# Kernel optimization log

Hardware: AMD Instinct MI355X
Metric: run time of the kernel (lower is better)

## Reference

```python
import jax, jax.numpy as jnp
import numpy as np

N, L, D = 4, 4096, 1024
H = 16
HD = D // H          # 64
MLP = 4 * D          # 4096
EPS = 1e-5

def log_g(x):
    # torch: where(x>=0, log(relu(x)+0.5), -softplus(-x))
    return jnp.where(x >= 0.0, jnp.log(jax.nn.relu(x) + 0.5), -jax.nn.softplus(-x))

def parallel_scan_log(log_coeffs, log_values):
    # log_coeffs: (B, L, C); log_values: (B, L+1, C)
    a_star = jnp.pad(jnp.cumsum(log_coeffs, axis=1), ((0, 0), (1, 0), (0, 0)))
    log_h = jax.lax.cumlogsumexp(log_values - a_star, axis=1)
    return jnp.exp(a_star[:, 1:] + log_h[:, 1:])

def layer_norm(x, gamma, beta):
    mu = jnp.mean(x, axis=-1, keepdims=True)
    var = jnp.var(x, axis=-1, keepdims=True)
    return (x - mu) * jax.lax.rsqrt(var + EPS) * gamma + beta

def setup_inputs() -> dict:
    key = jax.random.key(0)
    ks = jax.random.split(key, 12)
    s = 0.02
    return {
        "x": jax.random.normal(ks[0], (N, L, D), jnp.float32),
        "h_0": jax.random.normal(ks[1], (N, 1, D), jnp.float32),
        "w_in": jax.random.normal(ks[2], (D, D), jnp.float32) * s,
        "b_in": jnp.zeros((D,), jnp.float32),
        "wz": jax.random.normal(ks[3], (HD, HD), jnp.float32) * s,
        "bz": jnp.zeros((HD,), jnp.float32),
        "wh": jax.random.normal(ks[4], (HD, HD), jnp.float32) * s,
        "bh": jnp.zeros((HD,), jnp.float32),
        "w_out": jax.random.normal(ks[5], (D, D), jnp.float32) * s,
        "b_out": jnp.zeros((D,), jnp.float32),
        "ln1_g": jnp.ones((D,), jnp.float32),
        "ln1_b": jnp.zeros((D,), jnp.float32),
        "ln2_g": jnp.ones((D,), jnp.float32),
        "ln2_b": jnp.zeros((D,), jnp.float32),
        "mw1": jax.random.normal(ks[6], (D, MLP), jnp.float32) * s,
        "mb1": jnp.zeros((MLP,), jnp.float32),
        "mw2": jax.random.normal(ks[7], (MLP, MLP), jnp.float32) * s,
        "mb2": jnp.zeros((MLP,), jnp.float32),
        "mw3": jax.random.normal(ks[8], (MLP, D), jnp.float32) * s,
        "mb3": jnp.zeros((D,), jnp.float32),
    }

def reference(x, h_0, w_in, b_in, wz, bz, wh, bh, w_out, b_out,
              ln1_g, ln1_b, ln2_g, ln2_b, mw1, mb1, mw2, mb2, mw3, mb3):
    n, l, d = x.shape
    rnn_input = layer_norm(x, ln1_g, ln1_b)
    pi = rnn_input @ w_in + b_in                                 # (N,L,D)
    pi = pi.reshape(n, l, H, HD).transpose(0, 2, 1, 3).reshape(n * H, l, HD)
    h0 = h_0.reshape(n, 1, H, HD).transpose(0, 2, 1, 3).reshape(n * H, 1, HD)
    # minGRU in log-space
    k = pi @ wz + bz
    log_z = -jax.nn.softplus(-k)
    log_coeffs = -jax.nn.softplus(k)
    log_h0 = log_g(h0)
    log_th = log_g(pi @ wh + bh)
    h = parallel_scan_log(log_coeffs, jnp.concatenate([log_h0, log_z + log_th], axis=1))
    rnn_states = h.reshape(n, H, l, HD).transpose(0, 2, 1, 3).reshape(n, l, d)
    x = x + (rnn_states @ w_out + b_out)
    mlp_in = layer_norm(x, ln2_g, ln2_b)
    y = jax.nn.silu(mlp_in @ mw1 + mb1)
    y = jax.nn.silu(y @ mw2 + mb2)
    y = y @ mw3 + mb3
    return (x + y, rnn_states)
```

## Files before the change

### kernel.cpp

```cpp
#include <hip/hip_runtime.h>
#include <hip/hip_bf16.h>

typedef __attribute__((ext_vector_type(8))) short short8;
typedef __attribute__((ext_vector_type(4))) short short4v;
typedef __attribute__((ext_vector_type(4))) float f32x4;
using bf16 = __hip_bfloat16;

#define DEV static __device__ __forceinline__

DEV float bf2f(bf16 v) { return __bfloat162float(v); }
DEV bf16 f2bf(float v) { return __float2bfloat16(v); }
DEV float s2f(short s) {
  union { unsigned u; float f; } v;
  v.u = ((unsigned)(unsigned short)s) << 16;
  return v.f;
}
DEV short f2s(float v) {
  bf16 b = __float2bfloat16(v);
  return *(short*)&b;
}

DEV void gld_lds16(const void* g, void* l) {
  __builtin_amdgcn_global_load_lds(
      (const __attribute__((address_space(1))) void*)g,
      (__attribute__((address_space(3))) void*)l, 16, 0, 0);
}

__global__ __launch_bounds__(256)
void wconv_kernel(const float* __restrict__ w, bf16* __restrict__ wT, int K, int N) {
  __shared__ float tile[32][33];
  const int kt = blockIdx.x * 32, nt = blockIdx.y * 32;
  const int tx = threadIdx.x & 31, ty = threadIdx.x >> 5;
#pragma unroll
  for (int i = 0; i < 32; i += 8)
    tile[ty + i][tx] = w[(size_t)(kt + ty + i) * N + nt + tx];
  __syncthreads();
#pragma unroll
  for (int i = 0; i < 32; i += 8)
    wT[(size_t)(nt + ty + i) * K + kt + tx] = f2bf(tile[tx][ty + i]);
}

__global__ __launch_bounds__(256)
void ln_kernel(const float* __restrict__ x, const float* __restrict__ g,
               const float* __restrict__ b, bf16* __restrict__ out) {
  const int row = blockIdx.x;
  const int t = threadIdx.x;
  const float4 v = ((const float4*)(x + (size_t)row * 1024))[t];
  float s = v.x + v.y + v.z + v.w;
  float ss = v.x * v.x + v.y * v.y + v.z * v.z + v.w * v.w;
#pragma unroll
  for (int off = 32; off > 0; off >>= 1) {
    s += __shfl_down(s, off);
    ss += __shfl_down(ss, off);
  }
  __shared__ float red[8];
  if ((t & 63) == 0) { red[(t >> 6) * 2] = s; red[(t >> 6) * 2 + 1] = ss; }
  __syncthreads();
  s = red[0] + red[2] + red[4] + red[6];
  ss = red[1] + red[3] + red[5] + red[7];
  const float mu = s * (1.f / 1024.f);
  const float rstd = rsqrtf(ss * (1.f / 1024.f) - mu * mu + 1e-5f);
  const float4 g4 = ((const float4*)g)[t];
  const float4 b4 = ((const float4*)b)[t];
  struct alignas(8) B4 { bf16 v[4]; } o;
  o.v[0] = f2bf((v.x - mu) * rstd * g4.x + b4.x);
  o.v[1] = f2bf((v.y - mu) * rstd * g4.y + b4.y);
  o.v[2] = f2bf((v.z - mu) * rstd * g4.z + b4.z);
  o.v[3] = f2bf((v.w - mu) * rstd * g4.w + b4.w);
  *(B4*)(out + (size_t)row * 1024 + t * 4) = o;
}

template <int EPI>
__global__ __launch_bounds__(256, 2)
void gemm128(const bf16* __restrict__ A, const bf16* __restrict__ BT,
             const float* __restrict__ bias, const float* __restrict__ res,
             void* __restrict__ C, int M, int N, int K) {
  __shared__ short As[128 * 64];
  __shared__ short Bs[128 * 64];
  const int tid = threadIdx.x;
  const int l = tid & 63;
  const int w = tid >> 6;
  const int wr = w >> 1, wc = w & 1;

  const int nbn = N >> 7;
  const int nwg = gridDim.x;
  const int bid = blockIdx.x;
  const int q = nwg >> 3, r = nwg & 7;
  const int xcd = bid & 7, lin = bid >> 3;
  const int wg = (xcd < r ? xcd * (q + 1) : r * (q + 1) + (xcd - r) * q) + lin;
  const int bm = wg / nbn, bn = wg % nbn;

  const bf16* Ab = A + (size_t)bm * 128 * K;
  const bf16* Bb = BT + (size_t)bn * 128 * K;

  f32x4 acc[4][4];
#pragma unroll
  for (int i = 0; i < 4; ++i)
#pragma unroll
    for (int j = 0; j < 4; ++j) acc[i][j] = (f32x4){0.f, 0.f, 0.f, 0.f};

  const int srow = l >> 3;
  const int scol = (((l & 7) ^ (l >> 3)) << 3);

  for (int k0 = 0; k0 < K; k0 += 64) {
    __syncthreads();
#pragma unroll
    for (int p = 0; p < 4; ++p) {
      const int rowA = p * 32 + w * 8 + srow;
      gld_lds16(Ab + (size_t)rowA * K + k0 + scol, As + (p * 32 + w * 8) * 64);
      gld_lds16(Bb + (size_t)rowA * K + k0 + scol, Bs + (p * 32 + w * 8) * 64);
    }
    __syncthreads();
    const int xr = (l & 7) << 3;
#pragma unroll
    for (int kk = 0; kk < 2; ++kk) {
      short8 fa[4], fb[4];
#pragma unroll
      for (int m = 0; m < 4; ++m)
        fa[m] = *(const short8*)&As[(wr * 64 + m * 16 + (l & 15)) * 64 +
                                    ((kk * 32 + (l >> 4) * 8) ^ xr)];
#pragma unroll
      for (int n = 0; n < 4; ++n)
        fb[n] = *(const short8*)&Bs[(wc * 64 + n * 16 + (l & 15)) * 64 +
                                    ((kk * 32 + (l >> 4) * 8) ^ xr)];
#pragma unroll
      for (int m = 0; m < 4; ++m)
#pragma unroll
        for (int n = 0; n < 4; ++n)
          acc[m][n] = __builtin_amdgcn_mfma_f32_16x16x32_bf16(fa[m], fb[n], acc[m][n], 0, 0, 0);
    }
  }

  const int lc = l & 15;
  const int lr = (l >> 4) * 4;
#pragma unroll
  for (int m = 0; m < 4; ++m) {
    const int row = bm * 128 + wr * 64 + m * 16 + lr;
#pragma unroll
    for (int r2 = 0; r2 < 4; ++r2) {
      const size_t rowoff = (size_t)(row + r2) * N;
#pragma unroll
      for (int n = 0; n < 4; ++n) {
        const int col = bn * 128 + wc * 64 + n * 16 + lc;
        float v = acc[m][n][r2] + bias[col];
        const size_t off = rowoff + col;
        if constexpr (EPI == 1) v = v / (1.f + __expf(-v));
        if constexpr (EPI == 2) {
          ((float*)C)[off] = res[off] + v;
        } else {
          ((bf16*)C)[off] = f2bf(v);
        }
      }
    }
  }
  (void)M;
}

template <int EPI>
__global__ __launch_bounds__(512, 2)
void gemm256(const bf16* __restrict__ A, const bf16* __restrict__ BT,
             const float* __restrict__ bias, const float* __restrict__ res,
             void* __restrict__ C, int M, int N, int K) {
  __shared__ alignas(16) short As[2][256 * 64];
  __shared__ alignas(16) short Bs[2][256 * 64];
  const int tid = threadIdx.x;
  const int l = tid & 63;
  const int w = tid >> 6;
  const int wr = w >> 2;
  const int wc = w & 3;

  const int nbn = N >> 8;
  const int nwg = gridDim.x;
  const int bid = blockIdx.x;
  const int q = nwg >> 3, r = nwg & 7;
  const int xcd = bid & 7, lin = bid >> 3;
  const int wg = (xcd < r ? xcd * (q + 1) : r * (q + 1) + (xcd - r) * q) + lin;
  const int bm = wg / nbn, bn = wg % nbn;

  const bf16* Ab = A + (size_t)bm * 256 * K;
  const bf16* Bb = BT + (size_t)bn * 256 * K;

  const int gcol = ((l & 7) ^ (l >> 3)) << 3;
  const int fr = l & 15;
  const int kq = (l >> 4) << 3;
  const int xr = (l & 7) << 3;
  const int k0s = kq ^ xr;
  const int k1s = (32 + kq) ^ xr;

  const bf16* Abl = Ab + (size_t)(w * 16 + (l >> 3)) * K + gcol;
  const bf16* Bbl = Bb + (size_t)(w * 16 + (l >> 3)) * K + gcol;

  f32x4 acc[8][4];
#pragma unroll
  for (int i = 0; i < 8; ++i)
#pragma unroll
    for (int j = 0; j < 4; ++j) acc[i][j] = (f32x4){0.f, 0.f, 0.f, 0.f};

  short8 fa[2][2];
  short8 fb[4][2];

#define BARX() __builtin_amdgcn_s_barrier()
#define SBAR0() __builtin_amdgcn_sched_barrier(0)

#define STAGE_A(BUF, HALF, KT)                                                     \
  do {                                                                             \
    gld_lds16(Abl + (size_t)((HALF) * 128) * K + (size_t)(KT) * 64,                \
              &As[BUF][((HALF) * 128 + w * 16) * 64]);                             \
    gld_lds16(Abl + (size_t)((HALF) * 128 + 8) * K + (size_t)(KT) * 64,            \
              &As[BUF][((HALF) * 128 + w * 16 + 8) * 64]);                         \
  } while (0)

#define STAGE_B(BUF, HALF, KT)                                                     \
  do {                                                                             \
    gld_lds16(Bbl + (size_t)((HALF) * 128) * K + (size_t)(KT) * 64,                \
              &Bs[BUF][((HALF) * 128 + w * 16) * 64]);                             \
    gld_lds16(Bbl + (size_t)((HALF) * 128 + 8) * K + (size_t)(KT) * 64,            \
              &Bs[BUF][((HALF) * 128 + w * 16 + 8) * 64]);                         \
  } while (0)

#define RD_FA(BUF, Q)                                                                    \
  do {                                                                                  \
    fa[0][0] = *(const short8*)&As[BUF][(wr * 128 + (Q) * 32 + fr) * 64 + k0s];         \
    fa[0][1] = *(const short8*)&As[BUF][(wr * 128 + (Q) * 32 + fr) * 64 + k1s];         \
    fa[1][0] = *(const short8*)&As[BUF][(wr * 128 + (Q) * 32 + 16 + fr) * 64 + k0s];    \
    fa[1][1] = *(const short8*)&As[BUF][(wr * 128 + (Q) * 32 + 16 + fr) * 64 + k1s];    \
  } while (0)

#define RD_FB(BUF)                                                                      \
  do {                                                                                 \
    _Pragma("unroll") for (int n_ = 0; n_ < 4; ++n_) {                                 \
      fb[n_][0] = *(const short8*)&Bs[BUF][(wc * 64 + n_ * 16 + fr) * 64 + k0s];       \
      fb[n_][1] = *(const short8*)&Bs[BUF][(wc * 64 + n_ * 16 + fr) * 64 + k1s];       \
    }                                                                                  \
  } while (0)

#define MMA_Q(Q)                                                                        \
  do {                                                                                 \
    __builtin_amdgcn_s_setprio(1);                                                     \
    _Pragma("unroll") for (int n_ = 0; n_ < 4; ++n_) {                                 \
      acc[2 * (Q)][n_] = __builtin_amdgcn_mfma_f32_16x16x32_bf16(                      \
          fa[0][0], fb[n_][0], acc[2 * (Q)][n_], 0, 0, 0);                             \
      acc[2 * (Q) + 1][n_] = __builtin_amdgcn_mfma_f32_16x16x32_bf16(                  \
          fa[1][0], fb[n_][0], acc[2 * (Q) + 1][n_], 0, 0, 0);                         \
    }                                                                                  \
    _Pragma("unroll") for (int n_ = 0; n_ < 4; ++n_) {                                 \
      acc[2 * (Q)][n_] = __builtin_amdgcn_mfma_f32_16x16x32_bf16(                      \
          fa[0][1], fb[n_][1], acc[2 * (Q)][n_], 0, 0, 0);                             \
      acc[2 * (Q) + 1][n_] = __builtin_amdgcn_mfma_f32_16x16x32_bf16(                  \
          fa[1][1], fb[n_][1], acc[2 * (Q) + 1][n_], 0, 0, 0);                         \
    }                                                                                  \
    __builtin_amdgcn_s_setprio(0);                                                     \
  } while (0)

#define LGKM0() do { asm volatile("s_waitcnt lgkmcnt(0)"); SBAR0(); } while (0)

#define TILE(BUF, T, HASA, HASB)                                                       \
  do {                                                                                 \
                                                                               \
    LGKM0();                                                                           \
    MMA_Q(0);                                                                          \
    if (HASA) { STAGE_A((BUF) ^ 1, 0, (T) + 1); STAGE_A((BUF) ^ 1, 1, (T) + 1); }      \
    RD_FA(BUF, 1);                                                                     \
    SBAR0(); BARX();                                                                   \
                                                                               \
    LGKM0();                                                                           \
    MMA_Q(1);                                                                          \
    RD_FA(BUF, 2);                                                                     \
    SBAR0(); BARX();                                                                   \
                                                                               \
    LGKM0();                                                                           \
    MMA_Q(2);                                                                          \
    if (HASB) STAGE_B(BUF, 0, (T) + 2);                                                \
    if (HASA) {                                                                        \
      if (HASB) asm volatile("s_waitcnt vmcnt(2)" ::: "memory");                       \
      else      asm volatile("s_waitcnt vmcnt(0)" ::: "memory");                       \
    }                                                                                  \
    RD_FA(BUF, 3);                                                                     \
    SBAR0(); BARX();                                                                   \
                                                                               \
    LGKM0();                                                                           \
    MMA_Q(3);                                                                          \
    if (HASB) STAGE_B(BUF, 1, (T) + 2);                                                \
    if (HASA) {                                                                        \
      RD_FB((BUF) ^ 1);                                                                \
      RD_FA((BUF) ^ 1, 0);                                                             \
      SBAR0(); BARX();                                                                 \
    }                                                                                  \
  } while (0)

  STAGE_A(0, 0, 0); STAGE_A(0, 1, 0);
  STAGE_B(0, 0, 0); STAGE_B(0, 1, 0);
  STAGE_B(1, 0, 1); STAGE_B(1, 1, 1);
  asm volatile("s_waitcnt vmcnt(4)" ::: "memory");
  BARX();
  RD_FB(0);
  RD_FA(0, 0);

  const int NT = K >> 6;
  const int NI = NT >> 1;
#pragma unroll 1
  for (int i = 0; i < NI; ++i) {
    const int t0 = 2 * i;
    const bool b0 = (t0 + 2) < NT;
    const bool b1 = (t0 + 3) < NT;
    TILE(0, t0, true, b0);
    TILE(1, t0 + 1, b0, b1);
  }

#undef BARX
#undef SBAR0
#undef STAGE_A
#undef STAGE_B
#undef RD_FA
#undef RD_FB
#undef MMA_Q
#undef LGKM0
#undef TILE

  const int lc = l & 15;
  const int lr = (l >> 4) * 4;
#pragma unroll
  for (int m = 0; m < 8; ++m) {
    const int row = bm * 256 + wr * 128 + m * 16 + lr;
#pragma unroll
    for (int r2 = 0; r2 < 4; ++r2) {
      const size_t rowoff = (size_t)(row + r2) * N;
#pragma unroll
      for (int n = 0; n < 4; ++n) {
        const int col = bn * 256 + wc * 64 + n * 16 + lc;
        float v = acc[m][n][r2] + bias[col];
        const size_t off = rowoff + col;
        if constexpr (EPI == 1) v = v / (1.f + __expf(-v));
        if constexpr (EPI == 2) {
          ((float*)C)[off] = res[off] + v;
        } else {
          ((bf16*)C)[off] = f2bf(v);
        }
      }
    }
  }
  (void)M;
}

__global__ __launch_bounds__(256)
void heads_kernel(const bf16* __restrict__ piB,
                  const float* __restrict__ wz, const float* __restrict__ bz,
                  const float* __restrict__ wh, const float* __restrict__ bh,
                  bf16* __restrict__ aB, bf16* __restrict__ bB,
                  float* __restrict__ cA, float* __restrict__ cB) {
  __shared__ float wzs[4096], whs[4096], pis[4096];
  __shared__ float segA[4][64], segB[4][64];
  const int h = blockIdx.y;
  const int t0 = blockIdx.x * 64;
  const int tid = threadIdx.x;
#pragma unroll
  for (int i = tid; i < 4096; i += 256) {
    wzs[i] = wz[i];
    whs[i] = wh[i];
  }
#pragma unroll
  for (int rr = 0; rr < 4; ++rr) {
    const int v = tid + rr * 256;
    const int row = v >> 4, c4 = (v & 15) * 4;
    short4v p4 = *(const short4v*)(piB + (size_t)(t0 + row) * 1024 + h * 64 + c4);
    pis[row * 64 + c4 + 0] = s2f(p4[0]);
    pis[row * 64 + c4 + 1] = s2f(p4[1]);
    pis[row * 64 + c4 + 2] = s2f(p4[2]);
    pis[row * 64 + c4 + 3] = s2f(p4[3]);
  }
  __syncthreads();
  const int hd = tid & 63;
  const int tb = (tid >> 6) * 16;
  float accK[16], accT[16];
  const float bzv = bz[hd], bhv = bh[hd];
#pragma unroll
  for (int i = 0; i < 16; ++i) { accK[i] = bzv; accT[i] = bhv; }
  for (int j = 0; j < 64; ++j) {
    const float wzv = wzs[j * 64 + hd];
    const float whv = whs[j * 64 + hd];
#pragma unroll
    for (int i = 0; i < 16; ++i) {
      const float p = pis[(tb + i) * 64 + j];
      accK[i] = fmaf(p, wzv, accK[i]);
      accT[i] = fmaf(p, whv, accT[i]);
    }
  }
  float As = 1.f, Bs = 0.f;
#pragma unroll
  for (int i = 0; i < 16; ++i) {
    const float k = accK[i], th = accT[i];
    const float sig = 1.f / (1.f + __expf(-k));
    const float a = 1.f - sig;
    const float gg = th >= 0.f ? th + 0.5f : 1.f / (1.f + __expf(-th));
    const float bb = sig * gg;
    Bs = fmaf(a, Bs, bb);
    As *= a;
    const size_t idx = (size_t)(t0 + tb + i) * 1024 + h * 64 + hd;
    aB[idx] = f2bf(a);
    bB[idx] = f2bf(bb);
  }
  segA[tid >> 6][hd] = As;
  segB[tid >> 6][hd] = Bs;
  __syncthreads();
  if (tid < 64) {
    float A = segA[0][tid], B = segB[0][tid];
#pragma unroll
    for (int s = 1; s < 4; ++s) {
      B = fmaf(segA[s][tid], B, segB[s][tid]);
      A *= segA[s][tid];
    }
    const int n = t0 >> 12;
    const int chunk = (t0 >> 6) & 63;
    const size_t o = ((size_t)(n * 64 + chunk)) * 1024 + h * 64 + tid;
    cA[o] = A;
    cB[o] = B;
  }
}

__global__ __launch_bounds__(256)
void scan_phase2(const float* __restrict__ h0,
                 const float* __restrict__ cA, const float* __restrict__ cB,
                 float* __restrict__ hst) {
  const int idx = blockIdx.x * 256 + threadIdx.x;
  const int c = idx & 1023;
  const int n = idx >> 10;
  float hv = h0[(size_t)n * 1024 + c];
  hv = hv >= 0.f ? hv + 0.5f : 1.f / (1.f + __expf(-hv));
  for (int ch = 0; ch < 64; ++ch) {
    const size_t o = ((size_t)(n * 64 + ch)) * 1024 + c;
    hst[o] = hv;
    hv = fmaf(cA[o], hv, cB[o]);
  }
}

__global__ __launch_bounds__(128)
void scan_phase3(const bf16* __restrict__ aB, const bf16* __restrict__ bB,
                 const float* __restrict__ hst,
                 float* __restrict__ rnn, bf16* __restrict__ rnnB) {
  const int idx = blockIdx.x * 128 + threadIdx.x;
  const int c8 = idx & 127;
  const int chunk = (idx >> 7) & 63;
  const int n = idx >> 13;
  const int c0 = c8 * 8;
  float hv[8];
  const float4* hsrc = (const float4*)(hst + ((size_t)(n * 64 + chunk)) * 1024 + c0);
  float4 ha = hsrc[0], hb = hsrc[1];
  hv[0] = ha.x; hv[1] = ha.y; hv[2] = ha.z; hv[3] = ha.w;
  hv[4] = hb.x; hv[5] = hb.y; hv[6] = hb.z; hv[7] = hb.w;
  size_t base = ((size_t)(n * 4096 + chunk * 64)) * 1024 + c0;
#pragma unroll 4
  for (int s = 0; s < 64; ++s) {
    const short8 a8 = *(const short8*)(aB + base);
    const short8 b8 = *(const short8*)(bB + base);
    short8 ob;
    float4 o0, o1;
#pragma unroll
    for (int j = 0; j < 8; ++j) {
      hv[j] = fmaf(s2f(a8[j]), hv[j], s2f(b8[j]));
      ob[j] = f2s(hv[j]);
    }
    o0.x = hv[0]; o0.y = hv[1]; o0.z = hv[2]; o0.w = hv[3];
    o1.x = hv[4]; o1.y = hv[5]; o1.z = hv[6]; o1.w = hv[7];
    ((float4*)(rnn + base))[0] = o0;
    ((float4*)(rnn + base))[1] = o1;
    *(short8*)(rnnB + base) = ob;
    base += 1024;
  }
}

extern "C" void kernel_launch(void* const* d_in, const int* in_sizes, int n_in,
                              void* d_out, int out_size, void* d_ws, size_t ws_size,
                              hipStream_t stream) {
  const float* x    = (const float*)d_in[0];
  const float* h0   = (const float*)d_in[1];
  const float* w_in = (const float*)d_in[2];
  const float* b_in = (const float*)d_in[3];
  const float* wz   = (const float*)d_in[4];
  const float* bz   = (const float*)d_in[5];
  const float* wh   = (const float*)d_in[6];
  const float* bh   = (const float*)d_in[7];
  const float* w_out= (const float*)d_in[8];
  const float* b_out= (const float*)d_in[9];
  const float* ln1g = (const float*)d_in[10];
  const float* ln1b = (const float*)d_in[11];
  const float* ln2g = (const float*)d_in[12];
  const float* ln2b = (const float*)d_in[13];
  const float* mw1  = (const float*)d_in[14];
  const float* mb1  = (const float*)d_in[15];
  const float* mw2  = (const float*)d_in[16];
  const float* mb2  = (const float*)d_in[17];
  const float* mw3  = (const float*)d_in[18];
  const float* mb3  = (const float*)d_in[19];
  (void)in_sizes; (void)n_in; (void)out_size;

  float* out0 = (float*)d_out;
  float* out1 = (float*)d_out + (size_t)16384 * 1024;

  char* ws = (char*)d_ws;
  size_t o = 0;
  auto take = [&](size_t bytes) { char* p = ws + o; o += (bytes + 255) & ~(size_t)255; return p; };
  bf16* w_inT = (bf16*)take((size_t)1024 * 1024 * 2);
  bf16* w_outT= (bf16*)take((size_t)1024 * 1024 * 2);
  bf16* mw1T  = (bf16*)take((size_t)4096 * 1024 * 2);
  bf16* mw2T  = (bf16*)take((size_t)4096 * 4096 * 2);
  bf16* mw3T  = (bf16*)take((size_t)4096 * 1024 * 2);
  bf16* lnxB  = (bf16*)take((size_t)16384 * 1024 * 2);
  bf16* piB   = (bf16*)take((size_t)16384 * 1024 * 2);
  bf16* aB    = (bf16*)take((size_t)16384 * 1024 * 2);
  bf16* bB    = (bf16*)take((size_t)16384 * 1024 * 2);
  float* cA   = (float*)take((size_t)4 * 64 * 1024 * 4);
  float* cB   = (float*)take((size_t)4 * 64 * 1024 * 4);
  float* hst  = (float*)take((size_t)4 * 64 * 1024 * 4);
  if (o > ws_size) return;

  const size_t bigbuf = (size_t)16384 * 4096 * 2;
  bf16* t1 = aB;
  bf16* t2 = bB;
  bool big = false;
  if (o + 2 * bigbuf <= ws_size) {
    big = true;
    t1 = (bf16*)take(bigbuf);
    t2 = (bf16*)take(bigbuf);
  }

  wconv_kernel<<<dim3(32, 32), 256, 0, stream>>>(w_in, w_inT, 1024, 1024);
  wconv_kernel<<<dim3(32, 32), 256, 0, stream>>>(w_out, w_outT, 1024, 1024);
  wconv_kernel<<<dim3(32, 128), 256, 0, stream>>>(mw1, mw1T, 1024, 4096);
  wconv_kernel<<<dim3(128, 128), 256, 0, stream>>>(mw2, mw2T, 4096, 4096);
  wconv_kernel<<<dim3(128, 32), 256, 0, stream>>>(mw3, mw3T, 4096, 1024);

  ln_kernel<<<16384, 256, 0, stream>>>(x, ln1g, ln1b, lnxB);
  gemm256<0><<<256, 512, 0, stream>>>(lnxB, w_inT, b_in, nullptr, piB, 16384, 1024, 1024);

  heads_kernel<<<dim3(256, 16), 256, 0, stream>>>(piB, wz, bz, wh, bh, aB, bB, cA, cB);
  scan_phase2<<<16, 256, 0, stream>>>(h0, cA, cB, hst);
  scan_phase3<<<256, 128, 0, stream>>>(aB, bB, hst, out1, lnxB );

  gemm256<2><<<256, 512, 0, stream>>>(lnxB, w_outT, b_out, x, out0, 16384, 1024, 1024);

  ln_kernel<<<16384, 256, 0, stream>>>(out0, ln2g, ln2b, lnxB );
  if (big) {
    gemm256<1><<<1024, 512, 0, stream>>>(lnxB, mw1T, mb1, nullptr, t1, 16384, 4096, 1024);
    gemm256<1><<<1024, 512, 0, stream>>>(t1, mw2T, mb2, nullptr, t2, 16384, 4096, 4096);
    gemm128<2><<<1024, 256, 0, stream>>>(t2, mw3T, mb3, out0, out0, 16384, 1024, 4096);
  } else {
    for (int mc = 0; mc < 4; ++mc) {
      const bf16* a3 = lnxB + (size_t)mc * 4096 * 1024;
      gemm256<1><<<256, 512, 0, stream>>>(a3, mw1T, mb1, nullptr, t1, 4096, 4096, 1024);
      gemm256<1><<<256, 512, 0, stream>>>(t1, mw2T, mb2, nullptr, t2, 4096, 4096, 4096);
      float* oc = out0 + (size_t)mc * 4096 * 1024;
      gemm128<2><<<256, 256, 0, stream>>>(t2, mw3T, mb3, oc, oc, 4096, 1024, 4096);
    }
  }
}
```

Before: 1.191 ms.

## Triple-buffer A tiles in GEMM and transpose pi tile in heads kernel

The GEMM now keeps three LDS buffers for A and two for B. Prefetch runs two k-tiles ahead, with A staging spread across quarters and the loop unrolled in six-tile chunks. This is meant to hide global-load latency better, at the cost of 32 KB more LDS per block, which may reduce occupancy below the launch-bound target of 2 blocks per CU. The heads kernel also stores the pi tile transposed and padded so each thread reads 16 timesteps with four float4 LDS loads instead of 16 scalar loads. The new loop structure assumes the tile count fits the chunk and tail pattern, which may not hold for every K.

```diff
diff --git a/kernel.cpp b/kernel.cpp
--- a/kernel.cpp
+++ b/kernel.cpp
@@ -161,7 +161,7 @@
 void gemm256(const bf16* __restrict__ A, const bf16* __restrict__ BT,
              const float* __restrict__ bias, const float* __restrict__ res,
              void* __restrict__ C, int M, int N, int K) {
-  __shared__ alignas(16) short As[2][256 * 64];
+  __shared__ alignas(16) short As[3][256 * 64];
   __shared__ alignas(16) short Bs[2][256 * 64];
   const int tid = threadIdx.x;
   const int l = tid & 63;
@@ -202,19 +202,19 @@
 #define BARX() __builtin_amdgcn_s_barrier()
 #define SBAR0() __builtin_amdgcn_sched_barrier(0)
 
-#define STAGE_A(BUF, HALF, KT)                                                     \
+#define STAGE_A(BUF, HALF, P)                                                      \
   do {                                                                             \
-    gld_lds16(Abl + (size_t)((HALF) * 128) * K + (size_t)(KT) * 64,                \
+    gld_lds16((P) + (size_t)((HALF) * 128) * K,                                    \
               &As[BUF][((HALF) * 128 + w * 16) * 64]);                             \
-    gld_lds16(Abl + (size_t)((HALF) * 128 + 8) * K + (size_t)(KT) * 64,            \
+    gld_lds16((P) + (size_t)((HALF) * 128 + 8) * K,                                \
               &As[BUF][((HALF) * 128 + w * 16 + 8) * 64]);                         \
   } while (0)
 
-#define STAGE_B(BUF, HALF, KT)                                                     \
+#define STAGE_B(BUF, HALF, P)                                                      \
   do {                                                                             \
-    gld_lds16(Bbl + (size_t)((HALF) * 128) * K + (size_t)(KT) * 64,                \
+    gld_lds16((P) + (size_t)((HALF) * 128) * K,                                    \
               &Bs[BUF][((HALF) * 128 + w * 16) * 64]);                             \
-    gld_lds16(Bbl + (size_t)((HALF) * 128 + 8) * K + (size_t)(KT) * 64,            \
+    gld_lds16((P) + (size_t)((HALF) * 128 + 8) * K,                                \
               &Bs[BUF][((HALF) * 128 + w * 16 + 8) * 64]);                         \
   } while (0)
 
@@ -254,58 +254,69 @@
 
 #define LGKM0() do { asm volatile("s_waitcnt lgkmcnt(0)"); SBAR0(); } while (0)
 
-#define TILE(BUF, T, HASA, HASB)                                                       \
+#define TILE3(A0v, A1v, A2v, BSv, BTv, PF, NX)                                         \
   do {                                                                                 \
                                                                                \
     LGKM0();                                                                           \
     MMA_Q(0);                                                                          \
-    if (HASA) { STAGE_A((BUF) ^ 1, 0, (T) + 1); STAGE_A((BUF) ^ 1, 1, (T) + 1); }      \
-    RD_FA(BUF, 1);                                                                     \
+    if (PF) STAGE_A(A2v, 0, pfA);                                                      \
+    RD_FA(A0v, 1);                                                                     \
     SBAR0(); BARX();                                                                   \
                                                                                \
     LGKM0();                                                                           \
     MMA_Q(1);                                                                          \
-    RD_FA(BUF, 2);                                                                     \
+    if (PF) STAGE_A(A2v, 1, pfA);                                                      \
+    RD_FA(A0v, 2);                                                                     \
     SBAR0(); BARX();                                                                   \
                                                                                \
     LGKM0();                                                                           \
     MMA_Q(2);                                                                          \
-    if (HASB) STAGE_B(BUF, 0, (T) + 2);                                                \
-    if (HASA) {                                                                        \
-      if (HASB) asm volatile("s_waitcnt vmcnt(2)" ::: "memory");                       \
-      else      asm volatile("s_waitcnt vmcnt(0)" ::: "memory");                       \
+    if (PF) {                                                                          \
+      STAGE_B(BSv, 0, pfB);                                                            \
+      asm volatile("s_waitcnt vmcnt(6)" ::: "memory");                                 \
+    } else if (NX) {                                                                   \
+      asm volatile("s_waitcnt vmcnt(0)" ::: "memory");                                 \
     }                                                                                  \
-    RD_FA(BUF, 3);                                                                     \
+    RD_FA(A0v, 3);                                                                     \
     SBAR0(); BARX();                                                                   \
                                                                                \
     LGKM0();                                                                           \
     MMA_Q(3);                                                                          \
-    if (HASB) STAGE_B(BUF, 1, (T) + 2);                                                \
-    if (HASA) {                                                                        \
-      RD_FB((BUF) ^ 1);                                                                \
-      RD_FA((BUF) ^ 1, 0);                                                             \
+    if (PF) STAGE_B(BSv, 1, pfB);                                                      \
+    if (NX) {                                                                          \
+      RD_FB(BTv);                                                                      \
+      RD_FA(A1v, 0);                                                                   \
       SBAR0(); BARX();                                                                 \
     }                                                                                  \
+    if (PF) { pfA += 64; pfB += 64; }                                                  \
   } while (0)
 
-  STAGE_A(0, 0, 0); STAGE_A(0, 1, 0);
-  STAGE_B(0, 0, 0); STAGE_B(0, 1, 0);
-  STAGE_B(1, 0, 1); STAGE_B(1, 1, 1);
-  asm volatile("s_waitcnt vmcnt(4)" ::: "memory");
+  STAGE_A(0, 0, Abl); STAGE_A(0, 1, Abl);
+  STAGE_B(0, 0, Bbl); STAGE_B(0, 1, Bbl);
+  STAGE_A(1, 0, Abl + 64); STAGE_A(1, 1, Abl + 64);
+  STAGE_B(1, 0, Bbl + 64); STAGE_B(1, 1, Bbl + 64);
+  asm volatile("s_waitcnt vmcnt(8)" ::: "memory");
   BARX();
   RD_FB(0);
   RD_FA(0, 0);
 
   const int NT = K >> 6;
-  const int NI = NT >> 1;
+  const int nch = (NT - 4) / 6;
+  const bf16* pfA = Abl + 2 * 64;
+  const bf16* pfB = Bbl + 2 * 64;
 #pragma unroll 1
-  for (int i = 0; i < NI; ++i) {
-    const int t0 = 2 * i;
-    const bool b0 = (t0 + 2) < NT;
-    const bool b1 = (t0 + 3) < NT;
-    TILE(0, t0, true, b0);
-    TILE(1, t0 + 1, b0, b1);
-  }
+  for (int ch = 0; ch < nch; ++ch) {
+    TILE3(0, 1, 2, 0, 1, true, true);
+    TILE3(1, 2, 0, 1, 0, true, true);
+    TILE3(2, 0, 1, 0, 1, true, true);
+    TILE3(0, 1, 2, 1, 0, true, true);
+    TILE3(1, 2, 0, 0, 1, true, true);
+    TILE3(2, 0, 1, 1, 0, true, true);
+  }
+  TILE3(0, 1, 2, 0, 1, true, true);
+  TILE3(1, 2, 0, 1, 0, true, true);
+  TILE3(2, 0, 1, 0, 1, false, true);
+  TILE3(0, 1, 2, 1, 0, false, false);
 
 #undef BARX
 #undef SBAR0
@@ -315,7 +326,7 @@
 #undef RD_FB
 #undef MMA_Q
 #undef LGKM0
-#undef TILE
+#undef TILE3
 
   const int lc = l & 15;
   const int lr = (l >> 4) * 4;
@@ -348,7 +359,8 @@
                   const float* __restrict__ wh, const float* __restrict__ bh,
                   bf16* __restrict__ aB, bf16* __restrict__ bB,
                   float* __restrict__ cA, float* __restrict__ cB) {
-  __shared__ float wzs[4096], whs[4096], pis[4096];
+  __shared__ float wzs[4096], whs[4096];
+  __shared__ float pisT[64 * 68];
   __shared__ float segA[4][64], segB[4][64];
   const int h = blockIdx.y;
   const int t0 = blockIdx.x * 64;
@@ -363,10 +375,10 @@
     const int v = tid + rr * 256;
     const int row = v >> 4, c4 = (v & 15) * 4;
     short4v p4 = *(const short4v*)(piB + (size_t)(t0 + row) * 1024 + h * 64 + c4);
-    pis[row * 64 + c4 + 0] = s2f(p4[0]);
-    pis[row * 64 + c4 + 1] = s2f(p4[1]);
-    pis[row * 64 + c4 + 2] = s2f(p4[2]);
-    pis[row * 64 + c4 + 3] = s2f(p4[3]);
+    pisT[(c4 + 0) * 68 + row] = s2f(p4[0]);
+    pisT[(c4 + 1) * 68 + row] = s2f(p4[1]);
+    pisT[(c4 + 2) * 68 + row] = s2f(p4[2]);
+    pisT[(c4 + 3) * 68 + row] = s2f(p4[3]);
   }
   __syncthreads();
   const int hd = tid & 63;
@@ -378,11 +390,14 @@
   for (int j = 0; j < 64; ++j) {
     const float wzv = wzs[j * 64 + hd];
     const float whv = whs[j * 64 + hd];
+    const float4* pj = (const float4*)&pisT[j * 68 + tb];
+    const float4 p0 = pj[0], p1 = pj[1], p2 = pj[2], p3 = pj[3];
+    float p[16] = {p0.x, p0.y, p0.z, p0.w, p1.x, p1.y, p1.z, p1.w,
+                   p2.x, p2.y, p2.z, p2.w, p3.x, p3.y, p3.z, p3.w};
 #pragma unroll
     for (int i = 0; i < 16; ++i) {
-      const float p = pis[(tb + i) * 64 + j];
-      accK[i] = fmaf(p, wzv, accK[i]);
-      accT[i] = fmaf(p, whv, accT[i]);
+      accK[i] = fmaf(p[i], wzv, accK[i]);
+      accT[i] = fmaf(p[i], whv, accT[i]);
     }
   }
   float As = 1.f, Bs = 0.f;
```

Result: faster. 1.152 ms (-3.3%).
